# Performance work log

Measured on AMD Instinct MI355X. Metric: run time of the kernel, lower is better.

## Reference

```python
import jax, jax.numpy as jnp
import numpy as np

BATCH, N_IN, N_OUT = 1024, 512, 512
GRID, DEGREE = 8, 3
NUM_BASIS = GRID + DEGREE  # 11
LO, HI = -3.0, 3.0
_h = (HI - LO) / GRID
# extended knot vector: GRID + 2*DEGREE + 1 knots -> GRID + DEGREE basis functions
KNOTS = jnp.asarray(np.linspace(LO - DEGREE * _h, HI + DEGREE * _h,
                                GRID + 2 * DEGREE + 1), dtype=jnp.float32)


def bspline_basis(x):
    """Cox-de Boor recursion. x: (batch, n_in) -> (batch, n_in, NUM_BASIS)."""
    t = KNOTS
    xb = x[..., None]
    B = ((xb >= t[:-1]) & (xb < t[1:])).astype(x.dtype)  # degree 0
    for d in range(1, DEGREE + 1):
        left = (xb - t[:-(d + 1)]) / (t[d:-1] - t[:-(d + 1)])
        right = (t[d + 1:] - xb) / (t[d + 1:] - t[1:-d])
        B = left * B[..., :-1] + right * B[..., 1:]
    return B


def setup_inputs() -> dict:
    key = jax.random.key(0)
    kx, kc, kw = jax.random.split(key, 3)
    x = jax.random.normal(kx, (BATCH, N_IN), dtype=jnp.float32)
    # xavier_normal_ init for c: fan_in = num_basis, fan_out = n_in*n_out
    c_std = float(np.sqrt(2.0 / (N_IN * N_OUT + NUM_BASIS)))
    c = jax.random.normal(kc, (N_IN * N_OUT, NUM_BASIS), dtype=jnp.float32) * c_std
    w_std = float(np.sqrt(2.0 / (N_IN + N_OUT)))
    w = jax.random.normal(kw, (N_IN, N_OUT), dtype=jnp.float32) * w_std
    return {"x": x, "c": c, "w": w}


def reference(x, c, w):
    # spline basis: (batch, n_in, K)
    bx = bspline_basis(x)
    # per-edge coefficients: (n_in, n_out, K)
    cr = c.reshape(N_IN, N_OUT, NUM_BASIS)
    # out[b,i,o] = sum_k bx[b,i,k] * c[i,o,k]
    spline = jnp.einsum('bik,iok->bio', bx, cr)
    # w * (silu(x) + spline), summed over n_in -> (batch, n_out)
    out = jnp.einsum('io,bio->bo', w, jax.nn.silu(x)[..., None] + spline)
    return out
```

## Files before the change

### kernel.cpp

```cpp
#include <hip/hip_runtime.h>

#define BATCH 1024
#define NIN   512
#define NOUT  512
#define NB    11
#define KSPLINE (NIN * NB)
#define KDIM    (KSPLINE + NIN)
#define SPLITS  8
#define BK      32

typedef short bf16x8 __attribute__((ext_vector_type(8)));
typedef float f32x4  __attribute__((ext_vector_type(4)));

__device__ __forceinline__ unsigned short f2bf(float f) {
  unsigned u = __float_as_uint(f);
  u += 0x7fff + ((u >> 16) & 1);
  return (unsigned short)(u >> 16);
}

__global__ __launch_bounds__(256) void k_basis(const float* __restrict__ x,
                                               unsigned short* __restrict__ A) {
  int tid = blockIdx.x * 256 + threadIdx.x;
  float xv = x[tid];
  float B[14];
#pragma unroll
  for (int j = 0; j < 14; ++j) {
    float t0 = -5.25f + 0.75f * (float)j;
    float t1 = t0 + 0.75f;
    B[j] = (xv >= t0 && xv < t1) ? 1.0f : 0.0f;
  }
#pragma unroll
  for (int d = 1; d <= 3; ++d) {
    float inv = 1.0f / (0.75f * (float)d);
#pragma unroll
    for (int j = 0; j <= 13 - d; ++j) {
      float tj   = -5.25f + 0.75f * (float)j;
      float tjd1 = tj + 0.75f * (float)(d + 1);
      B[j] = (xv - tj) * inv * B[j] + (tjd1 - xv) * inv * B[j + 1];
    }
  }
  int b = tid >> 9, i = tid & 511;
  unsigned short* row = A + (size_t)b * KDIM;
#pragma unroll
  for (int j = 0; j < NB; ++j) row[i * NB + j] = f2bf(B[j]);
  float sig = 1.0f / (1.0f + __expf(-xv));
  row[KSPLINE + i] = f2bf(xv * sig);
}

__global__ __launch_bounds__(256) void k_coef(const float* __restrict__ c,
                                              const float* __restrict__ w,
                                              unsigned short* __restrict__ Bt) {
  int o  = blockIdx.x;
  int kk = blockIdx.y * 256 + threadIdx.x;
  float v;
  if (kk < KSPLINE) {
    int i = kk / NB;
    int k = kk - i * NB;
    v = c[(size_t)(i * NOUT + o) * NB + k] * w[i * NOUT + o];
  } else {
    int i = kk - KSPLINE;
    v = w[i * NOUT + o];
  }
  Bt[(size_t)o * KDIM + kk] = f2bf(v);
}

__global__ __launch_bounds__(256) void k_gemm(const unsigned short* __restrict__ A,
                                              const unsigned short* __restrict__ Bt,
                                              float* __restrict__ out,
                                              int kchunk) {
  __shared__ unsigned short As[128 * BK];
  __shared__ unsigned short Bs[128 * BK];
  const int tid  = threadIdx.x;
  const int lane = tid & 63, wave = tid >> 6;
  const int wr = wave >> 1, wc = wave & 1;
  const int mbase = blockIdx.x * 128, nbase = blockIdx.y * 128;
  const int split = blockIdx.z;
  const int k0 = split * kchunk;

  f32x4 acc[4][4] = {};

  const int mrow = lane & 15;
  const int kq   = (lane >> 4) * 8;

  for (int kk = k0; kk < k0 + kchunk; kk += BK) {
#pragma unroll
    for (int it = 0; it < 2; ++it) {
      int ch  = it * 256 + tid;
      int row = ch >> 2, col = (ch & 3) * 8;
      const unsigned short* ga = A  + (size_t)(mbase + row) * KDIM + kk + col;
      const unsigned short* gb = Bt + (size_t)(nbase + row) * KDIM + kk + col;
      unsigned short* la = As + (it * 256 + wave * 64) * 8;
      unsigned short* lb = Bs + (it * 256 + wave * 64) * 8;
      __builtin_amdgcn_global_load_lds((__attribute__((address_space(1))) const void*)ga,
                                       (__attribute__((address_space(3))) void*)la, 16, 0, 0);
      __builtin_amdgcn_global_load_lds((__attribute__((address_space(1))) const void*)gb,
                                       (__attribute__((address_space(3))) void*)lb, 16, 0, 0);
    }
    __syncthreads();

    bf16x8 af[4], bfr[4];
#pragma unroll
    for (int mt = 0; mt < 4; ++mt)
      af[mt] = *(const bf16x8*)&As[(wr * 64 + mt * 16 + mrow) * BK + kq];
#pragma unroll
    for (int nt = 0; nt < 4; ++nt)
      bfr[nt] = *(const bf16x8*)&Bs[(wc * 64 + nt * 16 + mrow) * BK + kq];
#pragma unroll
    for (int mt = 0; mt < 4; ++mt)
#pragma unroll
      for (int nt = 0; nt < 4; ++nt)
        acc[mt][nt] = __builtin_amdgcn_mfma_f32_16x16x32_bf16(af[mt], bfr[nt], acc[mt][nt], 0, 0, 0);
    __syncthreads();
  }

  const int rq = (lane >> 4) * 4;
#pragma unroll
  for (int mt = 0; mt < 4; ++mt)
#pragma unroll
    for (int nt = 0; nt < 4; ++nt) {
      int colg = nbase + wc * 64 + nt * 16 + mrow;
#pragma unroll
      for (int r = 0; r < 4; ++r) {
        int rowg = mbase + wr * 64 + mt * 16 + rq + r;
        out[((size_t)split * BATCH + rowg) * NOUT + colg] = acc[mt][nt][r];
      }
    }
}

__global__ __launch_bounds__(256) void k_reduce(const float* __restrict__ part,
                                                float* __restrict__ out) {
  int t = blockIdx.x * 256 + threadIdx.x;
  f32x4 s = ((const f32x4*)part)[t];
#pragma unroll
  for (int sp = 1; sp < SPLITS; ++sp)
    s += ((const f32x4*)part)[(size_t)sp * (BATCH * NOUT / 4) + t];
  ((f32x4*)out)[t] = s;
}

extern "C" void kernel_launch(void* const* d_in, const int* in_sizes, int n_in,
                              void* d_out, int out_size, void* d_ws, size_t ws_size,
                              hipStream_t stream) {
  const float* x = (const float*)d_in[0];
  const float* c = (const float*)d_in[1];
  const float* w = (const float*)d_in[2];
  float* out = (float*)d_out;

  unsigned short* A  = (unsigned short*)d_ws;
  unsigned short* Bt = A + (size_t)BATCH * KDIM;
  float* part = (float*)((char*)d_ws + ((size_t)BATCH + NOUT) * KDIM * 2);

  size_t need = ((size_t)BATCH + NOUT) * KDIM * 2 + (size_t)SPLITS * BATCH * NOUT * 4;

  k_basis<<<dim3((BATCH * NIN) / 256), 256, 0, stream>>>(x, A);
  k_coef<<<dim3(NOUT, KDIM / 256), 256, 0, stream>>>(c, w, Bt);
  if (ws_size >= need) {
    k_gemm<<<dim3(8, 4, SPLITS), 256, 0, stream>>>(A, Bt, part, KDIM / SPLITS);
    k_reduce<<<dim3((BATCH * NOUT / 4) / 256), 256, 0, stream>>>(part, out);
  } else {
    k_gemm<<<dim3(8, 4, 1), 256, 0, stream>>>(A, Bt, out, KDIM);
  }
}
```

Baseline: 106.0 us.

## Fuse B-spline basis into GEMM, coalesce coef prep, use bf16 split-K partials

Removes the separate basis kernel and its bf16 activation matrix. Each GEMM block now evaluates uniform cubic B-spline weights in closed form, plus silu, directly into LDS, with the K dimension padded to 12 per input. The coefficient prep kernel is rewritten to stage through shared memory for coalesced reads and writes. Split-K goes from 8 to 16, and partial sums are stored as bf16 to halve reduce traffic. The cost is extra rounding of the partials and per-iteration ALU work inside the GEMM, and the GEMM B loads now go through registers instead of direct global-to-LDS loads.

```diff
diff --git a/kernel.cpp b/kernel.cpp
--- a/kernel.cpp
+++ b/kernel.cpp
@@ -4,116 +4,162 @@
 #define NIN   512
 #define NOUT  512
 #define NB    11
-#define KSPLINE (NIN * NB)
-#define KDIM    (KSPLINE + NIN)
-#define SPLITS  8
-#define BK      32
+#define KDIM  (NIN * 12)
+#define SPLITS 16
+#define IPS    (NIN / SPLITS)
+#define LDW    104
 
 typedef short bf16x8 __attribute__((ext_vector_type(8)));
 typedef float f32x4  __attribute__((ext_vector_type(4)));
+typedef unsigned short ushort8 __attribute__((ext_vector_type(8)));
 
 __device__ __forceinline__ unsigned short f2bf(float f) {
   unsigned u = __float_as_uint(f);
   u += 0x7fff + ((u >> 16) & 1);
   return (unsigned short)(u >> 16);
 }
-
-__global__ __launch_bounds__(256) void k_basis(const float* __restrict__ x,
-                                               unsigned short* __restrict__ A) {
-  int tid = blockIdx.x * 256 + threadIdx.x;
-  float xv = x[tid];
-  float B[14];
-#pragma unroll
-  for (int j = 0; j < 14; ++j) {
-    float t0 = -5.25f + 0.75f * (float)j;
-    float t1 = t0 + 0.75f;
-    B[j] = (xv >= t0 && xv < t1) ? 1.0f : 0.0f;
-  }
-#pragma unroll
-  for (int d = 1; d <= 3; ++d) {
-    float inv = 1.0f / (0.75f * (float)d);
-#pragma unroll
-    for (int j = 0; j <= 13 - d; ++j) {
-      float tj   = -5.25f + 0.75f * (float)j;
-      float tjd1 = tj + 0.75f * (float)(d + 1);
-      B[j] = (xv - tj) * inv * B[j] + (tjd1 - xv) * inv * B[j + 1];
-    }
-  }
-  int b = tid >> 9, i = tid & 511;
-  unsigned short* row = A + (size_t)b * KDIM;
-#pragma unroll
-  for (int j = 0; j < NB; ++j) row[i * NB + j] = f2bf(B[j]);
-  float sig = 1.0f / (1.0f + __expf(-xv));
-  row[KSPLINE + i] = f2bf(xv * sig);
-}
-
-__global__ __launch_bounds__(256) void k_coef(const float* __restrict__ c,
+__device__ __forceinline__ float bf2f(unsigned short h) {
+  return __uint_as_float((unsigned)h << 16);
+}
+
+__global__ __launch_bounds__(256) void k_prep(const float* __restrict__ c,
                                               const float* __restrict__ w,
                                               unsigned short* __restrict__ Bt) {
-  int o  = blockIdx.x;
-  int kk = blockIdx.y * 256 + threadIdx.x;
-  float v;
-  if (kk < KSPLINE) {
-    int i = kk / NB;
-    int k = kk - i * NB;
-    v = c[(size_t)(i * NOUT + o) * NB + k] * w[i * NOUT + o];
-  } else {
-    int i = kk - KSPLINE;
-    v = w[i * NOUT + o];
-  }
-  Bt[(size_t)o * KDIM + kk] = f2bf(v);
-}
-
-__global__ __launch_bounds__(256) void k_gemm(const unsigned short* __restrict__ A,
-                                              const unsigned short* __restrict__ Bt,
-                                              float* __restrict__ out,
-                                              int kchunk) {
-  __shared__ unsigned short As[128 * BK];
-  __shared__ unsigned short Bs[128 * BK];
+  __shared__ float          ws_[8 * 128];
+  __shared__ unsigned short sbt[128 * 96];
+  int tid = threadIdx.x;
+  int bc  = blockIdx.x;
+  int i0  = (bc >> 2) * 8;
+  int o0  = (bc & 3) * 128;
+  {
+    int r = tid >> 5, oq = (tid & 31) * 4;
+    *(f32x4*)&ws_[r * 128 + oq] = *(const f32x4*)&w[(size_t)(i0 + r) * NOUT + o0 + oq];
+  }
+  __syncthreads();
+  for (int n = 0; n < 11; ++n) {
+    int ch  = n * 256 + tid;
+    int il  = ch / 352;
+    int off = (ch - il * 352) * 4;
+    f32x4 cv = *(const f32x4*)&c[(size_t)(i0 + il) * (NIN * NB) + (size_t)o0 * NB + off];
+#pragma unroll
+    for (int e = 0; e < 4; ++e) {
+      int t  = off + e;
+      int op = t / 11;
+      int k  = t - op * 11;
+      sbt[op * 96 + il * 12 + k] = f2bf(cv[e] * ws_[il * 128 + op]);
+    }
+  }
+  {
+    int il = tid >> 5, oq = (tid & 31) * 4;
+#pragma unroll
+    for (int e = 0; e < 4; ++e)
+      sbt[(oq + e) * 96 + il * 12 + 11] = f2bf(ws_[il * 128 + oq + e]);
+  }
+  __syncthreads();
+  for (int n = 0; n < 6; ++n) {
+    int ch = n * 256 + tid;
+    int op = ch / 12, q = ch - op * 12;
+    *(ushort8*)&Bt[(size_t)(o0 + op) * KDIM + i0 * 12 + q * 8] =
+        *(const ushort8*)&sbt[op * 96 + q * 8];
+  }
+}
+
+__global__ __launch_bounds__(256) void k_fused(const float* __restrict__ x,
+                                               const unsigned short* __restrict__ Bt,
+                                               unsigned short* __restrict__ part,
+                                               float* __restrict__ out,
+                                               int splits, int ipersplit) {
+  __shared__ unsigned short As[128 * LDW];
+  __shared__ unsigned short Bs[128 * LDW];
   const int tid  = threadIdx.x;
   const int lane = tid & 63, wave = tid >> 6;
   const int wr = wave >> 1, wc = wave & 1;
   const int mbase = blockIdx.x * 128, nbase = blockIdx.y * 128;
   const int split = blockIdx.z;
-  const int k0 = split * kchunk;
+  const int istart = split * ipersplit;
 
   f32x4 acc[4][4] = {};
-
   const int mrow = lane & 15;
   const int kq   = (lane >> 4) * 8;
 
-  for (int kk = k0; kk < k0 + kchunk; kk += BK) {
-#pragma unroll
-    for (int it = 0; it < 2; ++it) {
-      int ch  = it * 256 + tid;
-      int row = ch >> 2, col = (ch & 3) * 8;
-      const unsigned short* ga = A  + (size_t)(mbase + row) * KDIM + kk + col;
-      const unsigned short* gb = Bt + (size_t)(nbase + row) * KDIM + kk + col;
-      unsigned short* la = As + (it * 256 + wave * 64) * 8;
-      unsigned short* lb = Bs + (it * 256 + wave * 64) * 8;
-      __builtin_amdgcn_global_load_lds((__attribute__((address_space(1))) const void*)ga,
-                                       (__attribute__((address_space(3))) void*)la, 16, 0, 0);
-      __builtin_amdgcn_global_load_lds((__attribute__((address_space(1))) const void*)gb,
-                                       (__attribute__((address_space(3))) void*)lb, 16, 0, 0);
+  const int iters = ipersplit / 8;
+  for (int it = 0; it < iters; ++it) {
+    int ib = istart + it * 8;
+    {
+      int bl  = tid >> 1;
+      int il0 = (tid & 1) * 4;
+      f32x4 xv = *(const f32x4*)&x[(size_t)(mbase + bl) * NIN + ib + il0];
+      unsigned short* arow = &As[bl * LDW];
+#pragma unroll
+      for (int q = 0; q < 4; ++q) {
+        int col = (il0 + q) * 12;
+        *(unsigned long long*)&arow[col]     = 0ULL;
+        *(unsigned long long*)&arow[col + 4] = 0ULL;
+        *(unsigned long long*)&arow[col + 8] = 0ULL;
+        float xq = xv[q];
+        float um = (xq + 5.25f) * (1.0f / 0.75f);
+        int   m  = (int)floorf(um);
+        if (m >= 0 && m <= 13) {
+          float u  = um - (float)m;
+          float u2 = u * u, u3 = u2 * u;
+          float omu = 1.0f - u;
+          float w3 = u3 * (1.0f / 6.0f);
+          float w2 = (-3.0f*u3 + 3.0f*u2 + 3.0f*u + 1.0f) * (1.0f/6.0f);
+          float w1 = (3.0f*u3 - 6.0f*u2 + 4.0f) * (1.0f/6.0f);
+          float w0 = omu * omu * omu * (1.0f / 6.0f);
+          int j0 = m - 3;
+          if (j0 >= 0 && j0 <= 10)         arow[col + j0]     = f2bf(w0);
+          if (j0 + 1 >= 0 && j0 + 1 <= 10) arow[col + j0 + 1] = f2bf(w1);
+          if (j0 + 2 >= 0 && j0 + 2 <= 10) arow[col + j0 + 2] = f2bf(w2);
+          if (m <= 10)                     arow[col + m]      = f2bf(w3);
+        }
+        float sig = 1.0f / (1.0f + __expf(-xq));
+        arow[col + 11] = f2bf(xq * sig);
+      }
+    }
+#pragma unroll
+    for (int n = 0; n < 6; ++n) {
+      int ch  = n * 256 + tid;
+      int row = ch / 12;
+      int cg  = ch - row * 12;
+      ushort8 vb = *(const ushort8*)&Bt[(size_t)(nbase + row) * KDIM + ib * 12 + cg * 8];
+      *(ushort8*)&Bs[row * LDW + cg * 8] = vb;
     }
     __syncthreads();
 
-    bf16x8 af[4], bfr[4];
+#pragma unroll
+    for (int ks = 0; ks < 96; ks += 32) {
+      bf16x8 af[4], bfr[4];
+#pragma unroll
+      for (int mt = 0; mt < 4; ++mt)
+        af[mt] = *(const bf16x8*)&As[(wr * 64 + mt * 16 + mrow) * LDW + ks + kq];
+#pragma unroll
+      for (int nt = 0; nt < 4; ++nt)
+        bfr[nt] = *(const bf16x8*)&Bs[(wc * 64 + nt * 16 + mrow) * LDW + ks + kq];
+#pragma unroll
+      for (int mt = 0; mt < 4; ++mt)
+#pragma unroll
+        for (int nt = 0; nt < 4; ++nt)
+          acc[mt][nt] = __builtin_amdgcn_mfma_f32_16x16x32_bf16(af[mt], bfr[nt], acc[mt][nt], 0, 0, 0);
+    }
+    __syncthreads();
+  }
+
+  const int rq = (lane >> 4) * 4;
+  if (splits == 1) {
 #pragma unroll
     for (int mt = 0; mt < 4; ++mt)
-      af[mt] = *(const bf16x8*)&As[(wr * 64 + mt * 16 + mrow) * BK + kq];
-#pragma unroll
-    for (int nt = 0; nt < 4; ++nt)
-      bfr[nt] = *(const bf16x8*)&Bs[(wc * 64 + nt * 16 + mrow) * BK + kq];
-#pragma unroll
-    for (int mt = 0; mt < 4; ++mt)
-#pragma unroll
-      for (int nt = 0; nt < 4; ++nt)
-        acc[mt][nt] = __builtin_amdgcn_mfma_f32_16x16x32_bf16(af[mt], bfr[nt], acc[mt][nt], 0, 0, 0);
-    __syncthreads();
-  }
-
-  const int rq = (lane >> 4) * 4;
+#pragma unroll
+      for (int nt = 0; nt < 4; ++nt) {
+        int colg = nbase + wc * 64 + nt * 16 + mrow;
+#pragma unroll
+        for (int r = 0; r < 4; ++r) {
+          int rowg = mbase + wr * 64 + mt * 16 + rq + r;
+          out[(size_t)rowg * NOUT + colg] = acc[mt][nt][r];
+        }
+      }
+    return;
+  }
 #pragma unroll
   for (int mt = 0; mt < 4; ++mt)
 #pragma unroll
@@ -122,19 +168,26 @@
 #pragma unroll
       for (int r = 0; r < 4; ++r) {
         int rowg = mbase + wr * 64 + mt * 16 + rq + r;
-        out[((size_t)split * BATCH + rowg) * NOUT + colg] = acc[mt][nt][r];
+        part[((size_t)split * BATCH + rowg) * NOUT + colg] = f2bf(acc[mt][nt][r]);
       }
     }
 }
 
-__global__ __launch_bounds__(256) void k_reduce(const float* __restrict__ part,
+__global__ __launch_bounds__(256) void k_reduce(const unsigned short* __restrict__ part,
                                                 float* __restrict__ out) {
   int t = blockIdx.x * 256 + threadIdx.x;
-  f32x4 s = ((const f32x4*)part)[t];
-#pragma unroll
-  for (int sp = 1; sp < SPLITS; ++sp)
-    s += ((const f32x4*)part)[(size_t)sp * (BATCH * NOUT / 4) + t];
-  ((f32x4*)out)[t] = s;
+  const ushort8* pv = (const ushort8*)part;
+  float s[8] = {};
+#pragma unroll
+  for (int sp = 0; sp < SPLITS; ++sp) {
+    ushort8 v = pv[(size_t)sp * (BATCH * NOUT / 8) + t];
+#pragma unroll
+    for (int e = 0; e < 8; ++e) s[e] += bf2f(v[e]);
+  }
+  f32x4 lo = { s[0], s[1], s[2], s[3] };
+  f32x4 hi = { s[4], s[5], s[6], s[7] };
+  ((f32x4*)out)[t * 2]     = lo;
+  ((f32x4*)out)[t * 2 + 1] = hi;
 }
 
 extern "C" void kernel_launch(void* const* d_in, const int* in_sizes, int n_in,
@@ -145,18 +198,16 @@
   const float* w = (const float*)d_in[2];
   float* out = (float*)d_out;
 
-  unsigned short* A  = (unsigned short*)d_ws;
-  unsigned short* Bt = A + (size_t)BATCH * KDIM;
-  float* part = (float*)((char*)d_ws + ((size_t)BATCH + NOUT) * KDIM * 2);
-
-  size_t need = ((size_t)BATCH + NOUT) * KDIM * 2 + (size_t)SPLITS * BATCH * NOUT * 4;
-
-  k_basis<<<dim3((BATCH * NIN) / 256), 256, 0, stream>>>(x, A);
-  k_coef<<<dim3(NOUT, KDIM / 256), 256, 0, stream>>>(c, w, Bt);
+  unsigned short* Bt = (unsigned short*)d_ws;
+  size_t off_part = (size_t)NOUT * KDIM * 2;
+  unsigned short* part = (unsigned short*)((char*)d_ws + off_part);
+  size_t need = off_part + (size_t)SPLITS * BATCH * NOUT * 2;
+
+  k_prep<<<dim3(256), 256, 0, stream>>>(c, w, Bt);
   if (ws_size >= need) {
-    k_gemm<<<dim3(8, 4, SPLITS), 256, 0, stream>>>(A, Bt, part, KDIM / SPLITS);
-    k_reduce<<<dim3((BATCH * NOUT / 4) / 256), 256, 0, stream>>>(part, out);
+    k_fused<<<dim3(8, 4, SPLITS), 256, 0, stream>>>(x, Bt, part, out, SPLITS, IPS);
+    k_reduce<<<dim3((BATCH * NOUT / 8) / 256), 256, 0, stream>>>(part, out);
   } else {
-    k_gemm<<<dim3(8, 4, 1), 256, 0, stream>>>(A, Bt, out, KDIM);
-  }
-}
+    k_fused<<<dim3(8, 4, 1), 256, 0, stream>>>(x, Bt, part, out, 1, NIN);
+  }
+}
```

After: 92.46 us. 1.15x faster.
